# Kernel optimization log

Measured on AMD Instinct MI355X. Metric: run time of the kernel, lower is better.

Reference implementation:

```python
import jax, jax.numpy as jnp
import numpy as np

B, N, D = 2, 1024, 64
H, DK, DV = 4, 16, 16
DOUT = 128
STEPS = 3


def _ln(x, eps, w=None, b=None):
    mu = jnp.mean(x, axis=-1, keepdims=True)
    var = jnp.mean((x - mu) ** 2, axis=-1, keepdims=True)
    y = (x - mu) * jax.lax.rsqrt(var + eps)
    if w is not None:
        y = y * w + b
    return y


def setup_inputs() -> dict:
    key = jax.random.key(0)
    ks = jax.random.split(key, 16)
    q_x = jax.random.normal(ks[0], (B, N, D), jnp.float32)
    v_x = jax.random.normal(ks[1], (B, N, D), jnp.float32)
    qa = jax.random.uniform(ks[2], (B, N, N), jnp.float32)
    va = jax.random.uniform(ks[3], (B, N, N), jnp.float32)
    q_adj = qa / jnp.sum(qa, axis=-1, keepdims=True)  # row-normalized adjacency
    v_adj = va / jnp.sum(va, axis=-1, keepdims=True)
    s = 0.05
    w_qs = jax.random.normal(ks[4], (D, H * DK), jnp.float32) * s
    w_ks = jax.random.normal(ks[5], (D, H * DK), jnp.float32) * s
    w_vs = jax.random.normal(ks[6], (D, H * DV), jnp.float32) * s
    w_fc = jax.random.normal(ks[7], (H * DV, D), jnp.float32) * s
    mha_ln_w = jnp.ones((D,), jnp.float32)
    mha_ln_b = jnp.zeros((D,), jnp.float32)
    conv_w = jax.random.normal(ks[8], (D, DOUT), jnp.float32) * s
    conv_b = jnp.zeros((DOUT,), jnp.float32)
    lin_w = jax.random.normal(ks[9], (DOUT, D), jnp.float32) * s
    lin_b = jnp.zeros((D,), jnp.float32)
    norm_w = jnp.ones((D,), jnp.float32)
    norm_b = jnp.zeros((D,), jnp.float32)
    return dict(q_x=q_x, q_adj=q_adj, v_x=v_x, v_adj=v_adj,
                w_qs=w_qs, w_ks=w_ks, w_vs=w_vs, w_fc=w_fc,
                mha_ln_w=mha_ln_w, mha_ln_b=mha_ln_b,
                conv_w=conv_w, conv_b=conv_b, lin_w=lin_w, lin_b=lin_b,
                norm_w=norm_w, norm_b=norm_b)


def reference(q_x, q_adj, v_x, v_adj, w_qs, w_ks, w_vs, w_fc,
              mha_ln_w, mha_ln_b, conv_w, conv_b, lin_w, lin_b,
              norm_w, norm_b):
    b, n, d = q_x.shape
    residual = q_x
    qs, vs = [q_x], [v_x]
    q1 = jnp.einsum('bij,bjd->bid', q_adj, q_x)
    v1 = jnp.einsum('bij,bjd->bid', v_adj, v_x)
    qs.append(q1); vs.append(v1)
    for _ in range(2, STEPS):
        q1 = jnp.einsum('bij,bjd->bid', q_adj, q1)
        v1 = jnp.einsum('bij,bjd->bid', v_adj, v1)
        qs.append(q1); vs.append(v1)
    qc = _ln(jnp.concatenate(qs, axis=1), 1e-5)  # [b, STEPS*n, d]
    vc = _ln(jnp.concatenate(vs, axis=1), 1e-5)
    L = qc.shape[1]
    # multi-head attention (dropout = identity in eval)
    q = (qc @ w_qs).reshape(b, L, H, DK)
    k = (qc @ w_ks).reshape(b, L, H, DK)
    v = (vc @ w_vs).reshape(b, L, H, DV)
    scores = jnp.einsum('bqhd,bkhd->bhqk', q, k) / jnp.asarray(DK ** 0.5, q.dtype)
    attn = jax.nn.softmax(scores, axis=-1)
    o = jnp.einsum('bhqk,bkhd->bqhd', attn, v).reshape(b, L, H * DV)
    o = o @ w_fc + qc
    o = _ln(o, 1e-6, mha_ln_w, mha_ln_b)
    # pool across diffusion steps (faithful to original reshape semantics)
    x = jnp.mean(o.reshape(b, n, -1, STEPS), axis=-1)  # [b, n, d]
    x1 = jax.nn.relu(x @ conv_w + conv_b)
    x = residual + x1 @ lin_w + lin_b
    return _ln(x, 1e-5, norm_w, norm_b)
```

## Files before the change

kernel.cpp:

```cpp
#include <hip/hip_runtime.h>
#include <hip/hip_bf16.h>

#define B_ 2
#define N_ 1024
#define D_ 64
#define L_ 3072
#define H_ 4

typedef __attribute__((ext_vector_type(8))) short s8v;
typedef __attribute__((ext_vector_type(4))) short s4v;
typedef __attribute__((ext_vector_type(4))) float f32x4;

#define EXP2F(x) __builtin_amdgcn_exp2f(x)
#define QSCALE 0.36067376022224085f

__device__ __forceinline__ float wave_sum64(float v) {
#pragma unroll
    for (int off = 32; off > 0; off >>= 1) v += __shfl_xor(v, off, 64);
    return v;
}

__device__ __forceinline__ short f2bf(float f) {
    unsigned u = __float_as_uint(f);
    u += 0x7FFFu + ((u >> 16) & 1u);
    return (short)(u >> 16);
}

__device__ __forceinline__ s8v ldfrag_pad(const __hip_bfloat16* p) {
    s4v lo4 = *reinterpret_cast<const s4v*>(p);
    s8v r;
    r[0] = lo4[0]; r[1] = lo4[1]; r[2] = lo4[2]; r[3] = lo4[3];
    r[4] = 0; r[5] = 0; r[6] = 0; r[7] = 0;
    return r;
}
__device__ __forceinline__ s8v ldfrag_full(const __hip_bfloat16* p0, const __hip_bfloat16* p1) {
    s4v a = *reinterpret_cast<const s4v*>(p0);
    s4v b = *reinterpret_cast<const s4v*>(p1);
    s8v r;
    r[0] = a[0]; r[1] = a[1]; r[2] = a[2]; r[3] = a[3];
    r[4] = b[0]; r[5] = b[1]; r[6] = b[2]; r[7] = b[3];
    return r;
}
__device__ __forceinline__ s8v wfrag_build(const float* __restrict__ W, int N, int ct, int ks,
                                           int lo, int hi, float scale) {
    s8v r;
    int n = ct * 16 + lo;
    int k0 = ks * 32 + 4 * hi;
#pragma unroll
    for (int j = 0; j < 4; ++j) {
        r[j]     = f2bf(W[(k0 + j) * N + n] * scale);
        r[4 + j] = f2bf(W[(k0 + 16 + j) * N + n] * scale);
    }
    return r;
}

__global__ void xpose(const float* __restrict__ xq, const float* __restrict__ xv,
                      __hip_bfloat16* __restrict__ xtq, __hip_bfloat16* __restrict__ xtv) {
    __shared__ short ts[64][65];
    int m = blockIdx.y;
    int qv = m >> 1, b = m & 1;
    int l0 = blockIdx.x * 64;
    const float* x = (qv ? xv : xq) + (size_t)b * N_ * 64;
    int t = threadIdx.x;
#pragma unroll
    for (int i = 0; i < 4; ++i) {
        int f = t + i * 256;
        int r = f >> 4, c4 = f & 15;
        float4 v = *reinterpret_cast<const float4*>(x + (size_t)(l0 + r) * 64 + c4 * 4);
        ts[c4 * 4 + 0][r] = f2bf(v.x);
        ts[c4 * 4 + 1][r] = f2bf(v.y);
        ts[c4 * 4 + 2][r] = f2bf(v.z);
        ts[c4 * 4 + 3][r] = f2bf(v.w);
    }
    __syncthreads();
    short* xt = reinterpret_cast<short*>(qv ? xtv : xtq) + (size_t)b * 64 * N_;
#pragma unroll
    for (int i = 0; i < 4; ++i) {
        int f = t + i * 256;
        int d = f >> 4, seg = f & 15;
        s4v o;
        o[0] = ts[d][seg * 4 + 0]; o[1] = ts[d][seg * 4 + 1];
        o[2] = ts[d][seg * 4 + 2]; o[3] = ts[d][seg * 4 + 3];
        *reinterpret_cast<s4v*>(xt + (size_t)d * N_ + l0 + seg * 4) = o;
    }
}

__global__ __launch_bounds__(256) void spmm_mfma(
        const float* __restrict__ adj_q, const float* __restrict__ adj_v,
        const __hip_bfloat16* __restrict__ xtq, const __hip_bfloat16* __restrict__ xtv,
        float* __restrict__ oq, float* __restrict__ ov,
        __hip_bfloat16* __restrict__ oqt, __hip_bfloat16* __restrict__ ovt, int writet) {
    const int lane = threadIdx.x & 63;
    const int w = threadIdx.x >> 6;
    const int lo = lane & 15, hi = lane >> 4;
    const int rt = blockIdx.x;
    const int qv = blockIdx.y, b = blockIdx.z;

    const float* adj = (qv ? adj_v : adj_q) + (size_t)b * N_ * N_ + (size_t)(rt * 16 + lo) * N_;
    const __hip_bfloat16* xt = (qv ? xtv : xtq) + ((size_t)b * 64 + w * 16 + lo) * N_;

    f32x4 acc = {0.f, 0.f, 0.f, 0.f};
#pragma unroll 8
    for (int ks = 0; ks < 32; ++ks) {
        int k0 = ks * 32;
        float4 a4 = *reinterpret_cast<const float4*>(adj + k0 + 4 * hi);
        float4 b4 = *reinterpret_cast<const float4*>(adj + k0 + 16 + 4 * hi);
        s8v af;
        af[0] = f2bf(a4.x); af[1] = f2bf(a4.y); af[2] = f2bf(a4.z); af[3] = f2bf(a4.w);
        af[4] = f2bf(b4.x); af[5] = f2bf(b4.y); af[6] = f2bf(b4.z); af[7] = f2bf(b4.w);
        s8v xf = ldfrag_full(xt + k0 + 4 * hi, xt + k0 + 16 + 4 * hi);
        acc = __builtin_amdgcn_mfma_f32_16x16x32_bf16(xf, af, acc, 0, 0, 0);
    }
    float* o = (qv ? ov : oq) + ((size_t)b * N_ + rt * 16 + lo) * 64 + w * 16 + 4 * hi;
    *reinterpret_cast<f32x4*>(o) = acc;
    if (writet) {
        short* ot = reinterpret_cast<short*>(qv ? ovt : oqt) + (size_t)b * 64 * N_;
#pragma unroll
        for (int j = 0; j < 4; ++j)
            ot[(size_t)(w * 16 + 4 * hi + j) * N_ + rt * 16 + lo] = f2bf(acc[j]);
    }
}

__global__ void concat_ln(const float* __restrict__ qx, const float* __restrict__ q1,
                          const float* __restrict__ q2,
                          const float* __restrict__ vx, const float* __restrict__ v1,
                          const float* __restrict__ v2,
                          float* __restrict__ qc,
                          __hip_bfloat16* __restrict__ qcb, __hip_bfloat16* __restrict__ vcb) {
    int rid  = blockIdx.x * 4 + (threadIdx.x >> 6);
    int lane = threadIdx.x & 63;
    int qvsel = rid >= (B_ * L_);
    int r = qvsel ? rid - B_ * L_ : rid;
    int b = r / L_, l = r % L_;
    int s = l / N_, i = l % N_;
    const float* src;
    if (!qvsel) src = (s == 0) ? qx : (s == 1) ? q1 : q2;
    else        src = (s == 0) ? vx : (s == 1) ? v1 : v2;
    float v = src[((size_t)b * N_ + i) * D_ + lane];
    float mean = wave_sum64(v) * (1.0f / 64.0f);
    float d = v - mean;
    float var = wave_sum64(d * d) * (1.0f / 64.0f);
    float y = d * rsqrtf(var + 1e-5f);
    size_t o = ((size_t)b * L_ + l) * D_ + lane;
    if (!qvsel) {
        qc[o] = y;
        reinterpret_cast<short*>(qcb)[o] = f2bf(y);
    } else {
        reinterpret_cast<short*>(vcb)[o] = f2bf(y);
    }
}

__global__ __launch_bounds__(256) void gemm_qkv(
        const __hip_bfloat16* __restrict__ qcb, const __hip_bfloat16* __restrict__ vcb,
        const float* __restrict__ wq, const float* __restrict__ wk, const float* __restrict__ wv,
        __hip_bfloat16* __restrict__ qb, __hip_bfloat16* __restrict__ kb,
        __hip_bfloat16* __restrict__ vtb) {
    const int w = threadIdx.x >> 6;
    const int lane = threadIdx.x & 63;
    const int lo = lane & 15, hi = lane >> 4;
    const int ct0 = w * 3;

    s8v wf[3][2];
#pragma unroll
    for (int c = 0; c < 3; ++c) {
        int ct = ct0 + c;
        const float* W = (ct < 4) ? wq : (ct < 8) ? wk : wv;
        float sc = (ct < 4) ? QSCALE : 1.0f;
        wf[c][0] = wfrag_build(W, 64, ct & 3, 0, lo, hi, sc);
        wf[c][1] = wfrag_build(W, 64, ct & 3, 1, lo, hi, sc);
    }
    const bool needq = (ct0 < 8);
    const bool needv = (ct0 + 2 >= 8);
    const f32x4 zz = {0.f, 0.f, 0.f, 0.f};

#pragma unroll
    for (int rr = 0; rr < 2; ++rr) {
        int rt = blockIdx.x * 2 + rr;
        int rbase = rt * 16;
        int b = rbase / L_;
        int l = rbase % L_ + lo;
        s8v aq0, aq1, av0, av1;
        if (needq) {
            const __hip_bfloat16* ar = qcb + (size_t)(rbase + lo) * 64;
            aq0 = ldfrag_full(ar + 4 * hi, ar + 16 + 4 * hi);
            aq1 = ldfrag_full(ar + 32 + 4 * hi, ar + 48 + 4 * hi);
        }
        if (needv) {
            const __hip_bfloat16* ar = vcb + (size_t)(rbase + lo) * 64;
            av0 = ldfrag_full(ar + 4 * hi, ar + 16 + 4 * hi);
            av1 = ldfrag_full(ar + 32 + 4 * hi, ar + 48 + 4 * hi);
        }
#pragma unroll
        for (int c = 0; c < 3; ++c) {
            int ct = ct0 + c;
            f32x4 acc = zz;
            if (ct < 8) {
                acc = __builtin_amdgcn_mfma_f32_16x16x32_bf16(wf[c][0], aq0, acc, 0, 0, 0);
                acc = __builtin_amdgcn_mfma_f32_16x16x32_bf16(wf[c][1], aq1, acc, 0, 0, 0);
                __hip_bfloat16* dst = (ct < 4) ? qb : kb;
                int h = ct & 3;
                s4v o;
                o[0] = f2bf(acc[0]); o[1] = f2bf(acc[1]); o[2] = f2bf(acc[2]); o[3] = f2bf(acc[3]);
                *reinterpret_cast<s4v*>(reinterpret_cast<short*>(dst) +
                    ((size_t)(b * H_ + h) * L_ + l) * 16 + 4 * hi) = o;
            } else {
                acc = __builtin_amdgcn_mfma_f32_16x16x32_bf16(wf[c][0], av0, acc, 0, 0, 0);
                acc = __builtin_amdgcn_mfma_f32_16x16x32_bf16(wf[c][1], av1, acc, 0, 0, 0);
                int h = ct - 8;
                short* vt = reinterpret_cast<short*>(vtb);
#pragma unroll
                for (int j = 0; j < 4; ++j) {
                    int dv = 4 * hi + j;
                    vt[((size_t)(b * H_ + h) * 16 + dv) * L_ + l] = f2bf(acc[j]);
                }
            }
        }
    }
}

__global__ __launch_bounds__(256) void attn_mfma(
        const __hip_bfloat16* __restrict__ qb, const __hip_bfloat16* __restrict__ kb,
        const __hip_bfloat16* __restrict__ vtb, __hip_bfloat16* __restrict__ attnob) {
    const int lane = threadIdx.x & 63;
    const int w = threadIdx.x >> 6;
    const int g = blockIdx.x;
    const int bh = g / 96;
    const int tp = g % 96;
    const int b = bh >> 2, h = bh & 3;
    const int lo = lane & 15, hi = lane >> 4;
    const int q0 = tp * 32;

    const __hip_bfloat16* qbase = qb + (size_t)bh * L_ * 16;
    const __hip_bfloat16* kbase = kb + (size_t)bh * L_ * 16;
    const __hip_bfloat16* vtbase = vtb + ((size_t)bh * 16 + lo) * L_;

    s8v qfA = ldfrag_pad(qbase + (size_t)(q0 + lo) * 16 + 4 * hi);
    s8v qfB = ldfrag_pad(qbase + (size_t)(q0 + 16 + lo) * 16 + 4 * hi);

    f32x4 accA = {0.f, 0.f, 0.f, 0.f}, accB = {0.f, 0.f, 0.f, 0.f};
    float lsA = 0.f, lsB = 0.f;
    const f32x4 zz = {0.f, 0.f, 0.f, 0.f};

    const int kbeg = w * (L_ / 4), kend = kbeg + (L_ / 4);
    for (int kt = kbeg; kt < kend; kt += 32) {
        s8v kf0 = ldfrag_pad(kbase + (size_t)(kt + lo) * 16 + 4 * hi);
        s8v kf1 = ldfrag_pad(kbase + (size_t)(kt + 16 + lo) * 16 + 4 * hi);
        s8v vf  = ldfrag_full(vtbase + kt + 4 * hi, vtbase + kt + 16 + 4 * hi);

        f32x4 s0A = __builtin_amdgcn_mfma_f32_16x16x32_bf16(kf0, qfA, zz, 0, 0, 0);
        f32x4 s1A = __builtin_amdgcn_mfma_f32_16x16x32_bf16(kf1, qfA, zz, 0, 0, 0);
        f32x4 s0B = __builtin_amdgcn_mfma_f32_16x16x32_bf16(kf0, qfB, zz, 0, 0, 0);
        f32x4 s1B = __builtin_amdgcn_mfma_f32_16x16x32_bf16(kf1, qfB, zz, 0, 0, 0);

        float pA0 = EXP2F(s0A[0]), pA1 = EXP2F(s0A[1]), pA2 = EXP2F(s0A[2]), pA3 = EXP2F(s0A[3]);
        float pA4 = EXP2F(s1A[0]), pA5 = EXP2F(s1A[1]), pA6 = EXP2F(s1A[2]), pA7 = EXP2F(s1A[3]);
        float pB0 = EXP2F(s0B[0]), pB1 = EXP2F(s0B[1]), pB2 = EXP2F(s0B[2]), pB3 = EXP2F(s0B[3]);
        float pB4 = EXP2F(s1B[0]), pB5 = EXP2F(s1B[1]), pB6 = EXP2F(s1B[2]), pB7 = EXP2F(s1B[3]);
        lsA += ((pA0 + pA1) + (pA2 + pA3)) + ((pA4 + pA5) + (pA6 + pA7));
        lsB += ((pB0 + pB1) + (pB2 + pB3)) + ((pB4 + pB5) + (pB6 + pB7));

        s8v pfA, pfB;
        pfA[0] = f2bf(pA0); pfA[1] = f2bf(pA1); pfA[2] = f2bf(pA2); pfA[3] = f2bf(pA3);
        pfA[4] = f2bf(pA4); pfA[5] = f2bf(pA5); pfA[6] = f2bf(pA6); pfA[7] = f2bf(pA7);
        pfB[0] = f2bf(pB0); pfB[1] = f2bf(pB1); pfB[2] = f2bf(pB2); pfB[3] = f2bf(pB3);
        pfB[4] = f2bf(pB4); pfB[5] = f2bf(pB5); pfB[6] = f2bf(pB6); pfB[7] = f2bf(pB7);

        accA = __builtin_amdgcn_mfma_f32_16x16x32_bf16(vf, pfA, accA, 0, 0, 0);
        accB = __builtin_amdgcn_mfma_f32_16x16x32_bf16(vf, pfB, accB, 0, 0, 0);
    }

    lsA += __shfl_xor(lsA, 16, 64); lsA += __shfl_xor(lsA, 32, 64);
    lsB += __shfl_xor(lsB, 16, 64); lsB += __shfl_xor(lsB, 32, 64);

    __shared__ float red[4][2][64][5];
    red[w][0][lane][0] = accA[0]; red[w][0][lane][1] = accA[1];
    red[w][0][lane][2] = accA[2]; red[w][0][lane][3] = accA[3];
    red[w][0][lane][4] = lsA;
    red[w][1][lane][0] = accB[0]; red[w][1][lane][1] = accB[1];
    red[w][1][lane][2] = accB[2]; red[w][1][lane][3] = accB[3];
    red[w][1][lane][4] = lsB;
    __syncthreads();
    if (w < 2) {
        int t = w;
        float a0 = 0.f, a1 = 0.f, a2 = 0.f, a3 = 0.f, lt = 0.f;
#pragma unroll
        for (int ww = 0; ww < 4; ++ww) {
            a0 += red[ww][t][lane][0];
            a1 += red[ww][t][lane][1];
            a2 += red[ww][t][lane][2];
            a3 += red[ww][t][lane][3];
            lt += red[ww][t][lane][4];
        }
        float inv = 1.0f / lt;
        s4v o;
        o[0] = f2bf(a0 * inv); o[1] = f2bf(a1 * inv); o[2] = f2bf(a2 * inv); o[3] = f2bf(a3 * inv);
        *reinterpret_cast<s4v*>(reinterpret_cast<short*>(attnob) +
            ((size_t)b * L_ + q0 + t * 16 + lo) * 64 + h * 16 + 4 * hi) = o;
    }
}

__global__ __launch_bounds__(256) void gemm_fc_ln(
        const __hip_bfloat16* __restrict__ attnob, const float* __restrict__ qc,
        const float* __restrict__ wfc,
        const float* __restrict__ lnw, const float* __restrict__ lnb,
        float* __restrict__ o2) {
    const int rt = blockIdx.x * 4 + (threadIdx.x >> 6);
    const int lane = threadIdx.x & 63;
    const int lo = lane & 15, hi = lane >> 4;
    const f32x4 zz = {0.f, 0.f, 0.f, 0.f};

    s8v wf[4][2];
#pragma unroll
    for (int ct = 0; ct < 4; ++ct) {
        wf[ct][0] = wfrag_build(wfc, 64, ct, 0, lo, hi, 1.0f);
        wf[ct][1] = wfrag_build(wfc, 64, ct, 1, lo, hi, 1.0f);
    }
    const __hip_bfloat16* ar = attnob + (size_t)(rt * 16 + lo) * 64;
    s8v a0 = ldfrag_full(ar + 4 * hi, ar + 16 + 4 * hi);
    s8v a1 = ldfrag_full(ar + 32 + 4 * hi, ar + 48 + 4 * hi);

    f32x4 acc[4];
    const int row = rt * 16 + lo;
#pragma unroll
    for (int ct = 0; ct < 4; ++ct) {
        acc[ct] = zz;
        acc[ct] = __builtin_amdgcn_mfma_f32_16x16x32_bf16(wf[ct][0], a0, acc[ct], 0, 0, 0);
        acc[ct] = __builtin_amdgcn_mfma_f32_16x16x32_bf16(wf[ct][1], a1, acc[ct], 0, 0, 0);
        f32x4 rq = *reinterpret_cast<const f32x4*>(qc + (size_t)row * 64 + ct * 16 + 4 * hi);
        acc[ct][0] += rq[0]; acc[ct][1] += rq[1]; acc[ct][2] += rq[2]; acc[ct][3] += rq[3];
    }
    float s = 0.f;
#pragma unroll
    for (int ct = 0; ct < 4; ++ct) s += (acc[ct][0] + acc[ct][1]) + (acc[ct][2] + acc[ct][3]);
    s += __shfl_xor(s, 16, 64); s += __shfl_xor(s, 32, 64);
    float mean = s * (1.0f / 64.0f);
    float vs = 0.f;
#pragma unroll
    for (int ct = 0; ct < 4; ++ct) {
#pragma unroll
        for (int j = 0; j < 4; ++j) { float d = acc[ct][j] - mean; vs += d * d; }
    }
    vs += __shfl_xor(vs, 16, 64); vs += __shfl_xor(vs, 32, 64);
    float rsq = rsqrtf(vs * (1.0f / 64.0f) + 1e-6f);
#pragma unroll
    for (int ct = 0; ct < 4; ++ct) {
        f32x4 w4 = *reinterpret_cast<const f32x4*>(lnw + ct * 16 + 4 * hi);
        f32x4 b4 = *reinterpret_cast<const f32x4*>(lnb + ct * 16 + 4 * hi);
        f32x4 o;
#pragma unroll
        for (int j = 0; j < 4; ++j) o[j] = (acc[ct][j] - mean) * rsq * w4[j] + b4[j];
        *reinterpret_cast<f32x4*>(o2 + (size_t)row * 64 + ct * 16 + 4 * hi) = o;
    }
}

__global__ void pool_k(const float* __restrict__ o2, __hip_bfloat16* __restrict__ xb) {
    int rid  = blockIdx.x * 4 + (threadIdx.x >> 6);
    int lane = threadIdx.x & 63;
    int b = rid / N_, i = rid % N_;
    const float* ob = o2 + (size_t)b * L_ * 64 + (size_t)192 * i;
    int t = 3 * lane;
    float xv = (ob[t] + ob[t + 1] + ob[t + 2]) * (1.0f / 3.0f);
    reinterpret_cast<short*>(xb)[(size_t)rid * 64 + lane] = f2bf(xv);
}

__global__ __launch_bounds__(256) void gemm_conv(
        const __hip_bfloat16* __restrict__ xb, const float* __restrict__ convw,
        const float* __restrict__ convb, __hip_bfloat16* __restrict__ x1b) {
    const int w = threadIdx.x >> 6;
    const int lane = threadIdx.x & 63;
    const int lo = lane & 15, hi = lane >> 4;
    const int rt = blockIdx.x;
    const f32x4 zz = {0.f, 0.f, 0.f, 0.f};

    s8v wf[2][2];
#pragma unroll
    for (int c = 0; c < 2; ++c) {
        int ct = 2 * w + c;
        wf[c][0] = wfrag_build(convw, 128, ct, 0, lo, hi, 1.0f);
        wf[c][1] = wfrag_build(convw, 128, ct, 1, lo, hi, 1.0f);
    }
    const __hip_bfloat16* ar = xb + (size_t)(rt * 16 + lo) * 64;
    s8v a0 = ldfrag_full(ar + 4 * hi, ar + 16 + 4 * hi);
    s8v a1 = ldfrag_full(ar + 32 + 4 * hi, ar + 48 + 4 * hi);

#pragma unroll
    for (int c = 0; c < 2; ++c) {
        int ct = 2 * w + c;
        f32x4 acc = zz;
        acc = __builtin_amdgcn_mfma_f32_16x16x32_bf16(wf[c][0], a0, acc, 0, 0, 0);
        acc = __builtin_amdgcn_mfma_f32_16x16x32_bf16(wf[c][1], a1, acc, 0, 0, 0);
        f32x4 bia = *reinterpret_cast<const f32x4*>(convb + ct * 16 + 4 * hi);
        s4v o;
#pragma unroll
        for (int j = 0; j < 4; ++j) o[j] = f2bf(fmaxf(acc[j] + bia[j], 0.f));
        *reinterpret_cast<s4v*>(reinterpret_cast<short*>(x1b) +
            (size_t)(rt * 16 + lo) * 128 + ct * 16 + 4 * hi) = o;
    }
}

__global__ __launch_bounds__(256) void gemm_lin_ln(
        const __hip_bfloat16* __restrict__ x1b, const float* __restrict__ qx,
        const float* __restrict__ linw, const float* __restrict__ linb,
        const float* __restrict__ nw, const float* __restrict__ nb,
        float* __restrict__ out) {
    const int rt = blockIdx.x * 4 + (threadIdx.x >> 6);
    const int lane = threadIdx.x & 63;
    const int lo = lane & 15, hi = lane >> 4;
    const f32x4 zz = {0.f, 0.f, 0.f, 0.f};

    s8v wf[4][4];
#pragma unroll
    for (int ct = 0; ct < 4; ++ct)
#pragma unroll
        for (int ks = 0; ks < 4; ++ks)
            wf[ct][ks] = wfrag_build(linw, 64, ct, ks, lo, hi, 1.0f);

    const __hip_bfloat16* ar = x1b + (size_t)(rt * 16 + lo) * 128;
    s8v af[4];
#pragma unroll
    for (int ks = 0; ks < 4; ++ks)
        af[ks] = ldfrag_full(ar + ks * 32 + 4 * hi, ar + ks * 32 + 16 + 4 * hi);

    f32x4 acc[4];
    const int row = rt * 16 + lo;
#pragma unroll
    for (int ct = 0; ct < 4; ++ct) {
        acc[ct] = zz;
#pragma unroll
        for (int ks = 0; ks < 4; ++ks)
            acc[ct] = __builtin_amdgcn_mfma_f32_16x16x32_bf16(wf[ct][ks], af[ks], acc[ct], 0, 0, 0);
        f32x4 bia = *reinterpret_cast<const f32x4*>(linb + ct * 16 + 4 * hi);
        f32x4 rq  = *reinterpret_cast<const f32x4*>(qx + (size_t)row * 64 + ct * 16 + 4 * hi);
#pragma unroll
        for (int j = 0; j < 4; ++j) acc[ct][j] += bia[j] + rq[j];
    }
    float s = 0.f;
#pragma unroll
    for (int ct = 0; ct < 4; ++ct) s += (acc[ct][0] + acc[ct][1]) + (acc[ct][2] + acc[ct][3]);
    s += __shfl_xor(s, 16, 64); s += __shfl_xor(s, 32, 64);
    float mean = s * (1.0f / 64.0f);
    float vs = 0.f;
#pragma unroll
    for (int ct = 0; ct < 4; ++ct) {
#pragma unroll
        for (int j = 0; j < 4; ++j) { float d = acc[ct][j] - mean; vs += d * d; }
    }
    vs += __shfl_xor(vs, 16, 64); vs += __shfl_xor(vs, 32, 64);
    float rsq = rsqrtf(vs * (1.0f / 64.0f) + 1e-5f);
#pragma unroll
    for (int ct = 0; ct < 4; ++ct) {
        f32x4 w4 = *reinterpret_cast<const f32x4*>(nw + ct * 16 + 4 * hi);
        f32x4 b4 = *reinterpret_cast<const f32x4*>(nb + ct * 16 + 4 * hi);
        f32x4 o;
#pragma unroll
        for (int j = 0; j < 4; ++j) o[j] = (acc[ct][j] - mean) * rsq * w4[j] + b4[j];
        *reinterpret_cast<f32x4*>(out + (size_t)row * 64 + ct * 16 + 4 * hi) = o;
    }
}

extern "C" void kernel_launch(void* const* d_in, const int* in_sizes, int n_in,
                              void* d_out, int out_size, void* d_ws, size_t ws_size,
                              hipStream_t stream) {
    const float* q_x      = (const float*)d_in[0];
    const float* q_adj    = (const float*)d_in[1];
    const float* v_x      = (const float*)d_in[2];
    const float* v_adj    = (const float*)d_in[3];
    const float* w_qs     = (const float*)d_in[4];
    const float* w_ks     = (const float*)d_in[5];
    const float* w_vs     = (const float*)d_in[6];
    const float* w_fc     = (const float*)d_in[7];
    const float* mha_ln_w = (const float*)d_in[8];
    const float* mha_ln_b = (const float*)d_in[9];
    const float* conv_w   = (const float*)d_in[10];
    const float* conv_b   = (const float*)d_in[11];
    const float* lin_w    = (const float*)d_in[12];
    const float* lin_b    = (const float*)d_in[13];
    const float* norm_w   = (const float*)d_in[14];
    const float* norm_b   = (const float*)d_in[15];

    float* ws = (float*)d_ws;
    float* q1    = ws;
    float* v1    = q1 + 131072;
    float* q2    = v1 + 131072;
    float* v2    = q2 + 131072;
    float* qc    = v2 + 131072;
    float* o2    = qc + 393216;
    __hip_bfloat16* qcb    = (__hip_bfloat16*)(o2 + 393216);
    __hip_bfloat16* vcb    = qcb + 393216;
    __hip_bfloat16* qb     = vcb + 393216;
    __hip_bfloat16* kb     = qb + 393216;
    __hip_bfloat16* vtb    = kb + 393216;
    __hip_bfloat16* attnob = vtb + 393216;
    __hip_bfloat16* xtq    = attnob + 393216;
    __hip_bfloat16* xtv    = xtq + 131072;
    __hip_bfloat16* q1t    = xtv + 131072;
    __hip_bfloat16* v1t    = q1t + 131072;
    __hip_bfloat16* xb     = v1t + 131072;
    __hip_bfloat16* x1b    = xb + 131072;
    float* out   = (float*)d_out;

    xpose<<<dim3(16, 4), 256, 0, stream>>>(q_x, v_x, xtq, xtv);
    spmm_mfma<<<dim3(64, 2, 2), 256, 0, stream>>>(q_adj, v_adj, xtq, xtv,
                                                  q1, v1, q1t, v1t, 1);
    spmm_mfma<<<dim3(64, 2, 2), 256, 0, stream>>>(q_adj, v_adj, q1t, v1t,
                                                  q2, v2, nullptr, nullptr, 0);
    concat_ln<<<3072, 256, 0, stream>>>(q_x, q1, q2, v_x, v1, v2, qc, qcb, vcb);
    gemm_qkv<<<192, 256, 0, stream>>>(qcb, vcb, w_qs, w_ks, w_vs, qb, kb, vtb);
    attn_mfma<<<768, 256, 0, stream>>>(qb, kb, vtb, attnob);
    gemm_fc_ln<<<96, 256, 0, stream>>>(attnob, qc, w_fc, mha_ln_w, mha_ln_b, o2);
    pool_k<<<512, 256, 0, stream>>>(o2, xb);
    gemm_conv<<<128, 256, 0, stream>>>(xb, conv_w, conv_b, x1b);
    gemm_lin_ln<<<32, 256, 0, stream>>>(x1b, q_x, lin_w, lin_b, norm_w, norm_b, out);
}
```

Measured before the change: 177.0 us.

## Split-K waves in spmm and attention, prefetch K/V, use packed bf16 convert

The spmm kernel now runs 8 waves per block, with two K-halves per column tile whose partial sums are combined through shared memory. The attention kernel gives each wave a single 16-query tile and 8 waves per block, and prefetches the next K/V fragments one iteration ahead. Software bf16 rounding is replaced with the hardware v_cvt_pk_bf16_f32 instruction in several kernels. The aim is more parallelism on small grids and less conversion ALU work, at the cost of an extra LDS reduction and higher register and block pressure.

```diff
diff --git a/kernel.cpp b/kernel.cpp
--- a/kernel.cpp
+++ b/kernel.cpp
@@ -25,6 +25,13 @@
     u += 0x7FFFu + ((u >> 16) & 1u);
     return (short)(u >> 16);
 }
+__device__ __forceinline__ unsigned cvt_pk_bf16(float a, float b) {
+    unsigned r;
+    asm("v_cvt_pk_bf16_f32 %0, %1, %2" : "=v"(r) : "v"(a), "v"(b));
+    return r;
+}
+union pk8 { s8v v; unsigned u[4]; };
+union pk4 { s4v v; unsigned u[2]; };
 
 __device__ __forceinline__ s8v ldfrag_pad(const __hip_bfloat16* p) {
     s4v lo4 = *reinterpret_cast<const s4v*>(p);
@@ -85,39 +92,49 @@
     }
 }
 
-__global__ __launch_bounds__(256) void spmm_mfma(
+__global__ __launch_bounds__(512) void spmm_mfma(
         const float* __restrict__ adj_q, const float* __restrict__ adj_v,
         const __hip_bfloat16* __restrict__ xtq, const __hip_bfloat16* __restrict__ xtv,
         float* __restrict__ oq, float* __restrict__ ov,
         __hip_bfloat16* __restrict__ oqt, __hip_bfloat16* __restrict__ ovt, int writet) {
     const int lane = threadIdx.x & 63;
     const int w = threadIdx.x >> 6;
+    const int ct = w & 3, kh = w >> 2;
     const int lo = lane & 15, hi = lane >> 4;
     const int rt = blockIdx.x;
     const int qv = blockIdx.y, b = blockIdx.z;
 
     const float* adj = (qv ? adj_v : adj_q) + (size_t)b * N_ * N_ + (size_t)(rt * 16 + lo) * N_;
-    const __hip_bfloat16* xt = (qv ? xtv : xtq) + ((size_t)b * 64 + w * 16 + lo) * N_;
+    const __hip_bfloat16* xt = (qv ? xtv : xtq) + ((size_t)b * 64 + ct * 16 + lo) * N_;
 
     f32x4 acc = {0.f, 0.f, 0.f, 0.f};
-#pragma unroll 8
-    for (int ks = 0; ks < 32; ++ks) {
+#pragma unroll 4
+    for (int ks = kh * 16; ks < kh * 16 + 16; ++ks) {
         int k0 = ks * 32;
         float4 a4 = *reinterpret_cast<const float4*>(adj + k0 + 4 * hi);
         float4 b4 = *reinterpret_cast<const float4*>(adj + k0 + 16 + 4 * hi);
-        s8v af;
-        af[0] = f2bf(a4.x); af[1] = f2bf(a4.y); af[2] = f2bf(a4.z); af[3] = f2bf(a4.w);
-        af[4] = f2bf(b4.x); af[5] = f2bf(b4.y); af[6] = f2bf(b4.z); af[7] = f2bf(b4.w);
+        pk8 af;
+        af.u[0] = cvt_pk_bf16(a4.x, a4.y); af.u[1] = cvt_pk_bf16(a4.z, a4.w);
+        af.u[2] = cvt_pk_bf16(b4.x, b4.y); af.u[3] = cvt_pk_bf16(b4.z, b4.w);
         s8v xf = ldfrag_full(xt + k0 + 4 * hi, xt + k0 + 16 + 4 * hi);
-        acc = __builtin_amdgcn_mfma_f32_16x16x32_bf16(xf, af, acc, 0, 0, 0);
-    }
-    float* o = (qv ? ov : oq) + ((size_t)b * N_ + rt * 16 + lo) * 64 + w * 16 + 4 * hi;
-    *reinterpret_cast<f32x4*>(o) = acc;
-    if (writet) {
-        short* ot = reinterpret_cast<short*>(qv ? ovt : oqt) + (size_t)b * 64 * N_;
-#pragma unroll
-        for (int j = 0; j < 4; ++j)
-            ot[(size_t)(w * 16 + 4 * hi + j) * N_ + rt * 16 + lo] = f2bf(acc[j]);
+        acc = __builtin_amdgcn_mfma_f32_16x16x32_bf16(xf, af.v, acc, 0, 0, 0);
+    }
+    __shared__ float red[2][4][64][4];
+    red[kh][ct][lane][0] = acc[0]; red[kh][ct][lane][1] = acc[1];
+    red[kh][ct][lane][2] = acc[2]; red[kh][ct][lane][3] = acc[3];
+    __syncthreads();
+    if (kh == 0) {
+        f32x4 s;
+#pragma unroll
+        for (int j = 0; j < 4; ++j) s[j] = red[0][ct][lane][j] + red[1][ct][lane][j];
+        float* o = (qv ? ov : oq) + ((size_t)b * N_ + rt * 16 + lo) * 64 + ct * 16 + 4 * hi;
+        *reinterpret_cast<f32x4*>(o) = s;
+        if (writet) {
+            short* ot = reinterpret_cast<short*>(qv ? ovt : oqt) + (size_t)b * 64 * N_;
+#pragma unroll
+            for (int j = 0; j < 4; ++j)
+                ot[(size_t)(ct * 16 + 4 * hi + j) * N_ + rt * 16 + lo] = f2bf(s[j]);
+        }
     }
 }
 
@@ -199,10 +216,11 @@
                 acc = __builtin_amdgcn_mfma_f32_16x16x32_bf16(wf[c][1], aq1, acc, 0, 0, 0);
                 __hip_bfloat16* dst = (ct < 4) ? qb : kb;
                 int h = ct & 3;
-                s4v o;
-                o[0] = f2bf(acc[0]); o[1] = f2bf(acc[1]); o[2] = f2bf(acc[2]); o[3] = f2bf(acc[3]);
+                pk4 o;
+                o.u[0] = cvt_pk_bf16(acc[0], acc[1]);
+                o.u[1] = cvt_pk_bf16(acc[2], acc[3]);
                 *reinterpret_cast<s4v*>(reinterpret_cast<short*>(dst) +
-                    ((size_t)(b * H_ + h) * L_ + l) * 16 + 4 * hi) = o;
+                    ((size_t)(b * H_ + h) * L_ + l) * 16 + 4 * hi) = o.v;
             } else {
                 acc = __builtin_amdgcn_mfma_f32_16x16x32_bf16(wf[c][0], av0, acc, 0, 0, 0);
                 acc = __builtin_amdgcn_mfma_f32_16x16x32_bf16(wf[c][1], av1, acc, 0, 0, 0);
@@ -218,84 +236,80 @@
     }
 }
 
-__global__ __launch_bounds__(256) void attn_mfma(
+__global__ __launch_bounds__(512) void attn_mfma(
         const __hip_bfloat16* __restrict__ qb, const __hip_bfloat16* __restrict__ kb,
         const __hip_bfloat16* __restrict__ vtb, __hip_bfloat16* __restrict__ attnob) {
     const int lane = threadIdx.x & 63;
     const int w = threadIdx.x >> 6;
+    const int qt2 = w & 1, kg = w >> 1;
     const int g = blockIdx.x;
     const int bh = g / 96;
     const int tp = g % 96;
     const int b = bh >> 2, h = bh & 3;
     const int lo = lane & 15, hi = lane >> 4;
-    const int q0 = tp * 32;
+    const int q0 = tp * 32 + qt2 * 16;
 
     const __hip_bfloat16* qbase = qb + (size_t)bh * L_ * 16;
     const __hip_bfloat16* kbase = kb + (size_t)bh * L_ * 16;
     const __hip_bfloat16* vtbase = vtb + ((size_t)bh * 16 + lo) * L_;
 
-    s8v qfA = ldfrag_pad(qbase + (size_t)(q0 + lo) * 16 + 4 * hi);
-    s8v qfB = ldfrag_pad(qbase + (size_t)(q0 + 16 + lo) * 16 + 4 * hi);
-
-    f32x4 accA = {0.f, 0.f, 0.f, 0.f}, accB = {0.f, 0.f, 0.f, 0.f};
-    float lsA = 0.f, lsB = 0.f;
+    s8v qf = ldfrag_pad(qbase + (size_t)(q0 + lo) * 16 + 4 * hi);
+
+    f32x4 acc = {0.f, 0.f, 0.f, 0.f};
+    float ls = 0.f;
     const f32x4 zz = {0.f, 0.f, 0.f, 0.f};
 
-    const int kbeg = w * (L_ / 4), kend = kbeg + (L_ / 4);
+    const int kbeg = kg * (L_ / 4), kend = kbeg + (L_ / 4);
+    s8v kf0 = ldfrag_pad(kbase + (size_t)(kbeg + lo) * 16 + 4 * hi);
+    s8v kf1 = ldfrag_pad(kbase + (size_t)(kbeg + 16 + lo) * 16 + 4 * hi);
+    s8v vf  = ldfrag_full(vtbase + kbeg + 4 * hi, vtbase + kbeg + 16 + 4 * hi);
+
     for (int kt = kbeg; kt < kend; kt += 32) {
-        s8v kf0 = ldfrag_pad(kbase + (size_t)(kt + lo) * 16 + 4 * hi);
-        s8v kf1 = ldfrag_pad(kbase + (size_t)(kt + 16 + lo) * 16 + 4 * hi);
-        s8v vf  = ldfrag_full(vtbase + kt + 4 * hi, vtbase + kt + 16 + 4 * hi);
-
-        f32x4 s0A = __builtin_amdgcn_mfma_f32_16x16x32_bf16(kf0, qfA, zz, 0, 0, 0);
-        f32x4 s1A = __builtin_amdgcn_mfma_f32_16x16x32_bf16(kf1, qfA, zz, 0, 0, 0);
-        f32x4 s0B = __builtin_amdgcn_mfma_f32_16x16x32_bf16(kf0, qfB, zz, 0, 0, 0);
-        f32x4 s1B = __builtin_amdgcn_mfma_f32_16x16x32_bf16(kf1, qfB, zz, 0, 0, 0);
-
-        float pA0 = EXP2F(s0A[0]), pA1 = EXP2F(s0A[1]), pA2 = EXP2F(s0A[2]), pA3 = EXP2F(s0A[3]);
-        float pA4 = EXP2F(s1A[0]), pA5 = EXP2F(s1A[1]), pA6 = EXP2F(s1A[2]), pA7 = EXP2F(s1A[3]);
-        float pB0 = EXP2F(s0B[0]), pB1 = EXP2F(s0B[1]), pB2 = EXP2F(s0B[2]), pB3 = EXP2F(s0B[3]);
-        float pB4 = EXP2F(s1B[0]), pB5 = EXP2F(s1B[1]), pB6 = EXP2F(s1B[2]), pB7 = EXP2F(s1B[3]);
-        lsA += ((pA0 + pA1) + (pA2 + pA3)) + ((pA4 + pA5) + (pA6 + pA7));
-        lsB += ((pB0 + pB1) + (pB2 + pB3)) + ((pB4 + pB5) + (pB6 + pB7));
-
-        s8v pfA, pfB;
-        pfA[0] = f2bf(pA0); pfA[1] = f2bf(pA1); pfA[2] = f2bf(pA2); pfA[3] = f2bf(pA3);
-        pfA[4] = f2bf(pA4); pfA[5] = f2bf(pA5); pfA[6] = f2bf(pA6); pfA[7] = f2bf(pA7);
-        pfB[0] = f2bf(pB0); pfB[1] = f2bf(pB1); pfB[2] = f2bf(pB2); pfB[3] = f2bf(pB3);
-        pfB[4] = f2bf(pB4); pfB[5] = f2bf(pB5); pfB[6] = f2bf(pB6); pfB[7] = f2bf(pB7);
-
-        accA = __builtin_amdgcn_mfma_f32_16x16x32_bf16(vf, pfA, accA, 0, 0, 0);
-        accB = __builtin_amdgcn_mfma_f32_16x16x32_bf16(vf, pfB, accB, 0, 0, 0);
-    }
-
-    lsA += __shfl_xor(lsA, 16, 64); lsA += __shfl_xor(lsA, 32, 64);
-    lsB += __shfl_xor(lsB, 16, 64); lsB += __shfl_xor(lsB, 32, 64);
+        s8v ck0 = kf0, ck1 = kf1, cv = vf;
+        int nk = (kt + 32 < kend) ? kt + 32 : kbeg;
+        kf0 = ldfrag_pad(kbase + (size_t)(nk + lo) * 16 + 4 * hi);
+        kf1 = ldfrag_pad(kbase + (size_t)(nk + 16 + lo) * 16 + 4 * hi);
+        vf  = ldfrag_full(vtbase + nk + 4 * hi, vtbase + nk + 16 + 4 * hi);
+
+        f32x4 s0 = __builtin_amdgcn_mfma_f32_16x16x32_bf16(ck0, qf, zz, 0, 0, 0);
+        f32x4 s1 = __builtin_amdgcn_mfma_f32_16x16x32_bf16(ck1, qf, zz, 0, 0, 0);
+
+        float p0 = EXP2F(s0[0]), p1 = EXP2F(s0[1]), p2 = EXP2F(s0[2]), p3 = EXP2F(s0[3]);
+        float p4 = EXP2F(s1[0]), p5 = EXP2F(s1[1]), p6 = EXP2F(s1[2]), p7 = EXP2F(s1[3]);
+        ls += ((p0 + p1) + (p2 + p3)) + ((p4 + p5) + (p6 + p7));
+
+        pk8 pf;
+        pf.u[0] = cvt_pk_bf16(p0, p1); pf.u[1] = cvt_pk_bf16(p2, p3);
+        pf.u[2] = cvt_pk_bf16(p4, p5); pf.u[3] = cvt_pk_bf16(p6, p7);
+
+        acc = __builtin_amdgcn_mfma_f32_16x16x32_bf16(cv, pf.v, acc, 0, 0, 0);
+    }
+
+    ls += __shfl_xor(ls, 16, 64);
+    ls += __shfl_xor(ls, 32, 64);
 
     __shared__ float red[4][2][64][5];
-    red[w][0][lane][0] = accA[0]; red[w][0][lane][1] = accA[1];
-    red[w][0][lane][2] = accA[2]; red[w][0][lane][3] = accA[3];
-    red[w][0][lane][4] = lsA;
-    red[w][1][lane][0] = accB[0]; red[w][1][lane][1] = accB[1];
-    red[w][1][lane][2] = accB[2]; red[w][1][lane][3] = accB[3];
-    red[w][1][lane][4] = lsB;
+    red[kg][qt2][lane][0] = acc[0]; red[kg][qt2][lane][1] = acc[1];
+    red[kg][qt2][lane][2] = acc[2]; red[kg][qt2][lane][3] = acc[3];
+    red[kg][qt2][lane][4] = ls;
     __syncthreads();
     if (w < 2) {
         int t = w;
         float a0 = 0.f, a1 = 0.f, a2 = 0.f, a3 = 0.f, lt = 0.f;
 #pragma unroll
-        for (int ww = 0; ww < 4; ++ww) {
-            a0 += red[ww][t][lane][0];
-            a1 += red[ww][t][lane][1];
-            a2 += red[ww][t][lane][2];
-            a3 += red[ww][t][lane][3];
-            lt += red[ww][t][lane][4];
+        for (int g2 = 0; g2 < 4; ++g2) {
+            a0 += red[g2][t][lane][0];
+            a1 += red[g2][t][lane][1];
+            a2 += red[g2][t][lane][2];
+            a3 += red[g2][t][lane][3];
+            lt += red[g2][t][lane][4];
         }
         float inv = 1.0f / lt;
-        s4v o;
-        o[0] = f2bf(a0 * inv); o[1] = f2bf(a1 * inv); o[2] = f2bf(a2 * inv); o[3] = f2bf(a3 * inv);
+        pk4 o;
+        o.u[0] = cvt_pk_bf16(a0 * inv, a1 * inv);
+        o.u[1] = cvt_pk_bf16(a2 * inv, a3 * inv);
         *reinterpret_cast<s4v*>(reinterpret_cast<short*>(attnob) +
-            ((size_t)b * L_ + q0 + t * 16 + lo) * 64 + h * 16 + 4 * hi) = o;
+            ((size_t)b * L_ + tp * 32 + t * 16 + lo) * 64 + h * 16 + 4 * hi) = o.v;
     }
 }
 
@@ -390,11 +404,11 @@
         acc = __builtin_amdgcn_mfma_f32_16x16x32_bf16(wf[c][0], a0, acc, 0, 0, 0);
         acc = __builtin_amdgcn_mfma_f32_16x16x32_bf16(wf[c][1], a1, acc, 0, 0, 0);
         f32x4 bia = *reinterpret_cast<const f32x4*>(convb + ct * 16 + 4 * hi);
-        s4v o;
-#pragma unroll
-        for (int j = 0; j < 4; ++j) o[j] = f2bf(fmaxf(acc[j] + bia[j], 0.f));
+        pk4 o;
+        o.u[0] = cvt_pk_bf16(fmaxf(acc[0] + bia[0], 0.f), fmaxf(acc[1] + bia[1], 0.f));
+        o.u[1] = cvt_pk_bf16(fmaxf(acc[2] + bia[2], 0.f), fmaxf(acc[3] + bia[3], 0.f));
         *reinterpret_cast<s4v*>(reinterpret_cast<short*>(x1b) +
-            (size_t)(rt * 16 + lo) * 128 + ct * 16 + 4 * hi) = o;
+            (size_t)(rt * 16 + lo) * 128 + ct * 16 + 4 * hi) = o.v;
     }
 }
 
@@ -500,13 +514,13 @@
     float* out   = (float*)d_out;
 
     xpose<<<dim3(16, 4), 256, 0, stream>>>(q_x, v_x, xtq, xtv);
-    spmm_mfma<<<dim3(64, 2, 2), 256, 0, stream>>>(q_adj, v_adj, xtq, xtv,
+    spmm_mfma<<<dim3(64, 2, 2), 512, 0, stream>>>(q_adj, v_adj, xtq, xtv,
                                                   q1, v1, q1t, v1t, 1);
-    spmm_mfma<<<dim3(64, 2, 2), 256, 0, stream>>>(q_adj, v_adj, q1t, v1t,
+    spmm_mfma<<<dim3(64, 2, 2), 512, 0, stream>>>(q_adj, v_adj, q1t, v1t,
                                                   q2, v2, nullptr, nullptr, 0);
     concat_ln<<<3072, 256, 0, stream>>>(q_x, q1, q2, v_x, v1, v2, qc, qcb, vcb);
     gemm_qkv<<<192, 256, 0, stream>>>(qcb, vcb, w_qs, w_ks, w_vs, qb, kb, vtb);
-    attn_mfma<<<768, 256, 0, stream>>>(qb, kb, vtb, attnob);
+    attn_mfma<<<768, 512, 0, stream>>>(qb, kb, vtb, attnob);
     gemm_fc_ln<<<96, 256, 0, stream>>>(attnob, qc, w_fc, mha_ln_w, mha_ln_b, o2);
     pool_k<<<512, 256, 0, stream>>>(o2, xb);
     gemm_conv<<<128, 256, 0, stream>>>(xb, conv_w, conv_b, x1b);
```

New measurement: 193.4 us. 9.3% more time.

## Pack Q/K/V into per-lane MFMA fragment layout and use packed bf16 conversion

Applied to the files above, without the earlier changes.

gemm_qkv now writes Q, K and V directly in a fragment-packed layout, so each lane of the attention kernel loads one contiguous 16-byte s8v per 32-key tile instead of several strided 8-byte loads. The attention loop also software-prefetches the next K/V tile, using a wraparound index on the last iteration. Scalar round-to-nearest bf16 conversions are replaced with the hardware v_cvt_pk_bf16_f32 instruction across several kernels. In exchange, gemm_qkv gains more complex scattered stores for V, and the layout ties the producer and consumer kernels tightly together.

```diff
diff --git a/kernel.cpp b/kernel.cpp
--- a/kernel.cpp
+++ b/kernel.cpp
@@ -25,14 +25,14 @@
     u += 0x7FFFu + ((u >> 16) & 1u);
     return (short)(u >> 16);
 }
-
-__device__ __forceinline__ s8v ldfrag_pad(const __hip_bfloat16* p) {
-    s4v lo4 = *reinterpret_cast<const s4v*>(p);
-    s8v r;
-    r[0] = lo4[0]; r[1] = lo4[1]; r[2] = lo4[2]; r[3] = lo4[3];
-    r[4] = 0; r[5] = 0; r[6] = 0; r[7] = 0;
+__device__ __forceinline__ unsigned cvt_pk_bf16(float a, float b) {
+    unsigned r;
+    asm("v_cvt_pk_bf16_f32 %0, %1, %2" : "=v"(r) : "v"(a), "v"(b));
     return r;
 }
+union pk8 { s8v v; unsigned u[4]; };
+union pk4 { s4v v; unsigned u[2]; };
+
 __device__ __forceinline__ s8v ldfrag_full(const __hip_bfloat16* p0, const __hip_bfloat16* p1) {
     s4v a = *reinterpret_cast<const s4v*>(p0);
     s4v b = *reinterpret_cast<const s4v*>(p1);
@@ -105,11 +105,11 @@
         int k0 = ks * 32;
         float4 a4 = *reinterpret_cast<const float4*>(adj + k0 + 4 * hi);
         float4 b4 = *reinterpret_cast<const float4*>(adj + k0 + 16 + 4 * hi);
-        s8v af;
-        af[0] = f2bf(a4.x); af[1] = f2bf(a4.y); af[2] = f2bf(a4.z); af[3] = f2bf(a4.w);
-        af[4] = f2bf(b4.x); af[5] = f2bf(b4.y); af[6] = f2bf(b4.z); af[7] = f2bf(b4.w);
+        pk8 af;
+        af.u[0] = cvt_pk_bf16(a4.x, a4.y); af.u[1] = cvt_pk_bf16(a4.z, a4.w);
+        af.u[2] = cvt_pk_bf16(b4.x, b4.y); af.u[3] = cvt_pk_bf16(b4.z, b4.w);
         s8v xf = ldfrag_full(xt + k0 + 4 * hi, xt + k0 + 16 + 4 * hi);
-        acc = __builtin_amdgcn_mfma_f32_16x16x32_bf16(xf, af, acc, 0, 0, 0);
+        acc = __builtin_amdgcn_mfma_f32_16x16x32_bf16(xf, af.v, acc, 0, 0, 0);
     }
     float* o = (qv ? ov : oq) + ((size_t)b * N_ + rt * 16 + lo) * 64 + w * 16 + 4 * hi;
     *reinterpret_cast<f32x4*>(o) = acc;
@@ -153,8 +153,8 @@
 __global__ __launch_bounds__(256) void gemm_qkv(
         const __hip_bfloat16* __restrict__ qcb, const __hip_bfloat16* __restrict__ vcb,
         const float* __restrict__ wq, const float* __restrict__ wk, const float* __restrict__ wv,
-        __hip_bfloat16* __restrict__ qb, __hip_bfloat16* __restrict__ kb,
-        __hip_bfloat16* __restrict__ vtb) {
+        __hip_bfloat16* __restrict__ qpk, __hip_bfloat16* __restrict__ kpk,
+        __hip_bfloat16* __restrict__ vpk) {
     const int w = threadIdx.x >> 6;
     const int lane = threadIdx.x & 63;
     const int lo = lane & 15, hi = lane >> 4;
@@ -178,7 +178,9 @@
         int rt = blockIdx.x * 2 + rr;
         int rbase = rt * 16;
         int b = rbase / L_;
-        int l = rbase % L_ + lo;
+        int lloc = rbase % L_;
+        int t32 = lloc >> 5;
+        int half = (lloc >> 4) & 1;
         s8v aq0, aq1, av0, av1;
         if (needq) {
             const __hip_bfloat16* ar = qcb + (size_t)(rbase + lo) * 64;
@@ -197,21 +199,25 @@
             if (ct < 8) {
                 acc = __builtin_amdgcn_mfma_f32_16x16x32_bf16(wf[c][0], aq0, acc, 0, 0, 0);
                 acc = __builtin_amdgcn_mfma_f32_16x16x32_bf16(wf[c][1], aq1, acc, 0, 0, 0);
-                __hip_bfloat16* dst = (ct < 4) ? qb : kb;
                 int h = ct & 3;
-                s4v o;
-                o[0] = f2bf(acc[0]); o[1] = f2bf(acc[1]); o[2] = f2bf(acc[2]); o[3] = f2bf(acc[3]);
-                *reinterpret_cast<s4v*>(reinterpret_cast<short*>(dst) +
-                    ((size_t)(b * H_ + h) * L_ + l) * 16 + 4 * hi) = o;
+                int bh = b * H_ + h;
+                short* dst = reinterpret_cast<short*>((ct < 4) ? qpk : kpk);
+                pk4 o;
+                o.u[0] = cvt_pk_bf16(acc[0], acc[1]);
+                o.u[1] = cvt_pk_bf16(acc[2], acc[3]);
+                *reinterpret_cast<s4v*>(dst +
+                    (((size_t)bh * 96 + t32) * 64 + lane) * 8 + half * 4) = o.v;
             } else {
                 acc = __builtin_amdgcn_mfma_f32_16x16x32_bf16(wf[c][0], av0, acc, 0, 0, 0);
                 acc = __builtin_amdgcn_mfma_f32_16x16x32_bf16(wf[c][1], av1, acc, 0, 0, 0);
                 int h = ct - 8;
-                short* vt = reinterpret_cast<short*>(vtb);
+                int bh = b * H_ + h;
+                short* vt = reinterpret_cast<short*>(vpk);
+                size_t base = ((size_t)bh * 96 + t32) * 64 * 8;
 #pragma unroll
                 for (int j = 0; j < 4; ++j) {
-                    int dv = 4 * hi + j;
-                    vt[((size_t)(b * H_ + h) * 16 + dv) * L_ + l] = f2bf(acc[j]);
+                    int lanep = (lo >> 2) * 16 + (4 * hi + j);
+                    vt[base + (size_t)lanep * 8 + half * 4 + (lo & 3)] = f2bf(acc[j]);
                 }
             }
         }
@@ -219,33 +225,40 @@
 }
 
 __global__ __launch_bounds__(256) void attn_mfma(
-        const __hip_bfloat16* __restrict__ qb, const __hip_bfloat16* __restrict__ kb,
-        const __hip_bfloat16* __restrict__ vtb, __hip_bfloat16* __restrict__ attnob) {
+        const __hip_bfloat16* __restrict__ qpk, const __hip_bfloat16* __restrict__ kpk,
+        const __hip_bfloat16* __restrict__ vpk, __hip_bfloat16* __restrict__ attnob) {
     const int lane = threadIdx.x & 63;
-    const int w = threadIdx.x >> 6;
+    const int kg = threadIdx.x >> 6;
     const int g = blockIdx.x;
     const int bh = g / 96;
     const int tp = g % 96;
     const int b = bh >> 2, h = bh & 3;
     const int lo = lane & 15, hi = lane >> 4;
-    const int q0 = tp * 32;
-
-    const __hip_bfloat16* qbase = qb + (size_t)bh * L_ * 16;
-    const __hip_bfloat16* kbase = kb + (size_t)bh * L_ * 16;
-    const __hip_bfloat16* vtbase = vtb + ((size_t)bh * 16 + lo) * L_;
-
-    s8v qfA = ldfrag_pad(qbase + (size_t)(q0 + lo) * 16 + 4 * hi);
-    s8v qfB = ldfrag_pad(qbase + (size_t)(q0 + 16 + lo) * 16 + 4 * hi);
+
+    const s8v* kp = reinterpret_cast<const s8v*>(kpk) + ((size_t)bh * 96) * 64 + lane;
+    const s8v* vp = reinterpret_cast<const s8v*>(vpk) + ((size_t)bh * 96) * 64 + lane;
+    const s8v* qp = reinterpret_cast<const s8v*>(qpk) + ((size_t)bh * 96 + tp) * 64 + lane;
+
+    s8v q8 = *qp;
+    s8v qfA = {q8[0], q8[1], q8[2], q8[3], 0, 0, 0, 0};
+    s8v qfB = {q8[4], q8[5], q8[6], q8[7], 0, 0, 0, 0};
 
     f32x4 accA = {0.f, 0.f, 0.f, 0.f}, accB = {0.f, 0.f, 0.f, 0.f};
     float lsA = 0.f, lsB = 0.f;
     const f32x4 zz = {0.f, 0.f, 0.f, 0.f};
 
-    const int kbeg = w * (L_ / 4), kend = kbeg + (L_ / 4);
-    for (int kt = kbeg; kt < kend; kt += 32) {
-        s8v kf0 = ldfrag_pad(kbase + (size_t)(kt + lo) * 16 + 4 * hi);
-        s8v kf1 = ldfrag_pad(kbase + (size_t)(kt + 16 + lo) * 16 + 4 * hi);
-        s8v vf  = ldfrag_full(vtbase + kt + 4 * hi, vtbase + kt + 16 + 4 * hi);
+    const int t0 = kg * 24, t1 = t0 + 24;
+    s8v kf8 = kp[(size_t)t0 * 64];
+    s8v vf8 = vp[(size_t)t0 * 64];
+
+    for (int t = t0; t < t1; ++t) {
+        s8v ck = kf8, cv = vf8;
+        int nt = (t + 1 < t1) ? t + 1 : t0;
+        kf8 = kp[(size_t)nt * 64];
+        vf8 = vp[(size_t)nt * 64];
+
+        s8v kf0 = {ck[0], ck[1], ck[2], ck[3], 0, 0, 0, 0};
+        s8v kf1 = {ck[4], ck[5], ck[6], ck[7], 0, 0, 0, 0};
 
         f32x4 s0A = __builtin_amdgcn_mfma_f32_16x16x32_bf16(kf0, qfA, zz, 0, 0, 0);
         f32x4 s1A = __builtin_amdgcn_mfma_f32_16x16x32_bf16(kf1, qfA, zz, 0, 0, 0);
@@ -259,43 +272,44 @@
         lsA += ((pA0 + pA1) + (pA2 + pA3)) + ((pA4 + pA5) + (pA6 + pA7));
         lsB += ((pB0 + pB1) + (pB2 + pB3)) + ((pB4 + pB5) + (pB6 + pB7));
 
-        s8v pfA, pfB;
-        pfA[0] = f2bf(pA0); pfA[1] = f2bf(pA1); pfA[2] = f2bf(pA2); pfA[3] = f2bf(pA3);
-        pfA[4] = f2bf(pA4); pfA[5] = f2bf(pA5); pfA[6] = f2bf(pA6); pfA[7] = f2bf(pA7);
-        pfB[0] = f2bf(pB0); pfB[1] = f2bf(pB1); pfB[2] = f2bf(pB2); pfB[3] = f2bf(pB3);
-        pfB[4] = f2bf(pB4); pfB[5] = f2bf(pB5); pfB[6] = f2bf(pB6); pfB[7] = f2bf(pB7);
-
-        accA = __builtin_amdgcn_mfma_f32_16x16x32_bf16(vf, pfA, accA, 0, 0, 0);
-        accB = __builtin_amdgcn_mfma_f32_16x16x32_bf16(vf, pfB, accB, 0, 0, 0);
+        pk8 pfA, pfB;
+        pfA.u[0] = cvt_pk_bf16(pA0, pA1); pfA.u[1] = cvt_pk_bf16(pA2, pA3);
+        pfA.u[2] = cvt_pk_bf16(pA4, pA5); pfA.u[3] = cvt_pk_bf16(pA6, pA7);
+        pfB.u[0] = cvt_pk_bf16(pB0, pB1); pfB.u[1] = cvt_pk_bf16(pB2, pB3);
+        pfB.u[2] = cvt_pk_bf16(pB4, pB5); pfB.u[3] = cvt_pk_bf16(pB6, pB7);
+
+        accA = __builtin_amdgcn_mfma_f32_16x16x32_bf16(cv, pfA.v, accA, 0, 0, 0);
+        accB = __builtin_amdgcn_mfma_f32_16x16x32_bf16(cv, pfB.v, accB, 0, 0, 0);
     }
 
     lsA += __shfl_xor(lsA, 16, 64); lsA += __shfl_xor(lsA, 32, 64);
     lsB += __shfl_xor(lsB, 16, 64); lsB += __shfl_xor(lsB, 32, 64);
 
     __shared__ float red[4][2][64][5];
-    red[w][0][lane][0] = accA[0]; red[w][0][lane][1] = accA[1];
-    red[w][0][lane][2] = accA[2]; red[w][0][lane][3] = accA[3];
-    red[w][0][lane][4] = lsA;
-    red[w][1][lane][0] = accB[0]; red[w][1][lane][1] = accB[1];
-    red[w][1][lane][2] = accB[2]; red[w][1][lane][3] = accB[3];
-    red[w][1][lane][4] = lsB;
+    red[kg][0][lane][0] = accA[0]; red[kg][0][lane][1] = accA[1];
+    red[kg][0][lane][2] = accA[2]; red[kg][0][lane][3] = accA[3];
+    red[kg][0][lane][4] = lsA;
+    red[kg][1][lane][0] = accB[0]; red[kg][1][lane][1] = accB[1];
+    red[kg][1][lane][2] = accB[2]; red[kg][1][lane][3] = accB[3];
+    red[kg][1][lane][4] = lsB;
     __syncthreads();
-    if (w < 2) {
-        int t = w;
+    if (kg < 2) {
+        int t = kg;
         float a0 = 0.f, a1 = 0.f, a2 = 0.f, a3 = 0.f, lt = 0.f;
 #pragma unroll
-        for (int ww = 0; ww < 4; ++ww) {
-            a0 += red[ww][t][lane][0];
-            a1 += red[ww][t][lane][1];
-            a2 += red[ww][t][lane][2];
-            a3 += red[ww][t][lane][3];
-            lt += red[ww][t][lane][4];
+        for (int g2 = 0; g2 < 4; ++g2) {
+            a0 += red[g2][t][lane][0];
+            a1 += red[g2][t][lane][1];
+            a2 += red[g2][t][lane][2];
+            a3 += red[g2][t][lane][3];
+            lt += red[g2][t][lane][4];
         }
         float inv = 1.0f / lt;
-        s4v o;
-        o[0] = f2bf(a0 * inv); o[1] = f2bf(a1 * inv); o[2] = f2bf(a2 * inv); o[3] = f2bf(a3 * inv);
+        pk4 o;
+        o.u[0] = cvt_pk_bf16(a0 * inv, a1 * inv);
+        o.u[1] = cvt_pk_bf16(a2 * inv, a3 * inv);
         *reinterpret_cast<s4v*>(reinterpret_cast<short*>(attnob) +
-            ((size_t)b * L_ + q0 + t * 16 + lo) * 64 + h * 16 + 4 * hi) = o;
+            ((size_t)b * L_ + tp * 32 + t * 16 + lo) * 64 + h * 16 + 4 * hi) = o.v;
     }
 }
 
@@ -390,11 +404,11 @@
         acc = __builtin_amdgcn_mfma_f32_16x16x32_bf16(wf[c][0], a0, acc, 0, 0, 0);
         acc = __builtin_amdgcn_mfma_f32_16x16x32_bf16(wf[c][1], a1, acc, 0, 0, 0);
         f32x4 bia = *reinterpret_cast<const f32x4*>(convb + ct * 16 + 4 * hi);
-        s4v o;
-#pragma unroll
-        for (int j = 0; j < 4; ++j) o[j] = f2bf(fmaxf(acc[j] + bia[j], 0.f));
+        pk4 o;
+        o.u[0] = cvt_pk_bf16(fmaxf(acc[0] + bia[0], 0.f), fmaxf(acc[1] + bia[1], 0.f));
+        o.u[1] = cvt_pk_bf16(fmaxf(acc[2] + bia[2], 0.f), fmaxf(acc[3] + bia[3], 0.f));
         *reinterpret_cast<s4v*>(reinterpret_cast<short*>(x1b) +
-            (size_t)(rt * 16 + lo) * 128 + ct * 16 + 4 * hi) = o;
+            (size_t)(rt * 16 + lo) * 128 + ct * 16 + 4 * hi) = o.v;
     }
 }
 
@@ -487,10 +501,10 @@
     float* o2    = qc + 393216;
     __hip_bfloat16* qcb    = (__hip_bfloat16*)(o2 + 393216);
     __hip_bfloat16* vcb    = qcb + 393216;
-    __hip_bfloat16* qb     = vcb + 393216;
-    __hip_bfloat16* kb     = qb + 393216;
-    __hip_bfloat16* vtb    = kb + 393216;
-    __hip_bfloat16* attnob = vtb + 393216;
+    __hip_bfloat16* qpk    = vcb + 393216;
+    __hip_bfloat16* kpk    = qpk + 393216;
+    __hip_bfloat16* vpk    = kpk + 393216;
+    __hip_bfloat16* attnob = vpk + 393216;
     __hip_bfloat16* xtq    = attnob + 393216;
     __hip_bfloat16* xtv    = xtq + 131072;
     __hip_bfloat16* q1t    = xtv + 131072;
@@ -505,8 +519,8 @@
     spmm_mfma<<<dim3(64, 2, 2), 256, 0, stream>>>(q_adj, v_adj, q1t, v1t,
                                                   q2, v2, nullptr, nullptr, 0);
     concat_ln<<<3072, 256, 0, stream>>>(q_x, q1, q2, v_x, v1, v2, qc, qcb, vcb);
-    gemm_qkv<<<192, 256, 0, stream>>>(qcb, vcb, w_qs, w_ks, w_vs, qb, kb, vtb);
-    attn_mfma<<<768, 256, 0, stream>>>(qb, kb, vtb, attnob);
+    gemm_qkv<<<192, 256, 0, stream>>>(qcb, vcb, w_qs, w_ks, w_vs, qpk, kpk, vpk);
+    attn_mfma<<<768, 256, 0, stream>>>(qpk, kpk, vpk, attnob);
     gemm_fc_ln<<<96, 256, 0, stream>>>(attnob, qc, w_fc, mha_ln_w, mha_ln_b, o2);
     pool_k<<<512, 256, 0, stream>>>(o2, xb);
     gemm_conv<<<128, 256, 0, stream>>>(xb, conv_w, conv_b, x1b);
```

After: 168.9 us. -4.6%, faster.
